# Kernel tuning notes

Hardware: AMD Instinct MI355X
Metric: run time of the kernel (lower is better)

The kernel has to match this reference:

```python
import jax, jax.numpy as jnp
import numpy as np

N_FLUID, N_BOX, K_MAX, KS, NCELL = 6000, 3000, 80, 4, 64
RADIUS = np.float32(0.5 * 1.5 * 6 * 0.025)  # filter_extent / 2 = 0.1125


def _ball_to_cube(p):
    """Volume-preserving ball->cube mapping (open3d ContinuousConv convention).
    p: [..., 3] coordinates in the unit ball; returns coords in [-1,1]^3."""
    eps = 1e-12
    x, y, z = p[..., 0], p[..., 1], p[..., 2]
    sq = x * x + y * y + z * z
    norm = jnp.sqrt(sq)
    rxy2 = x * x + y * y
    # sphere -> cylinder (volume preserving)
    polar = 1.25 * z * z > rxy2
    s_pol = jnp.sqrt(3.0 * norm / (norm + jnp.abs(z) + eps))
    s_eq = norm / jnp.sqrt(rxy2 + eps)
    xc = jnp.where(polar, s_pol * x, s_eq * x)
    yc = jnp.where(polar, s_pol * y, s_eq * y)
    zc = jnp.where(polar, jnp.sign(z) * norm, 1.5 * z * s_eq)
    zero = sq < 1e-12
    xc = jnp.where(zero, 0.0, xc)
    yc = jnp.where(zero, 0.0, yc)
    zc = jnp.where(zero, 0.0, zc)
    # cylinder -> cube (area-preserving disc -> square on xy)
    rxy = jnp.sqrt(xc * xc + yc * yc)
    FP = 4.0 / np.pi
    safe_x = jnp.where(jnp.abs(xc) < eps, eps, xc)
    safe_y = jnp.where(jnp.abs(yc) < eps, eps, yc)
    cond = jnp.abs(xc) >= jnp.abs(yc)
    u1 = jnp.sign(xc) * rxy
    v1 = u1 * FP * jnp.arctan(yc / safe_x)
    v2 = jnp.sign(yc) * rxy
    u2 = v2 * FP * jnp.arctan(xc / safe_y)
    u = jnp.where(cond, u1, u2)
    v = jnp.where(cond, v1, v2)
    small = rxy < eps
    u = jnp.where(small, 0.0, u)
    v = jnp.where(small, 0.0, v)
    return jnp.stack([u, v, zc], axis=-1)


def build_neighbors(pos_in, pos_out, ignore_self):
    """Fixed-radius neighbor search (capped at K_MAX) + window + trilinear
    interpolation cells/weights. Returns idx [No,K], cells [No,K,8] int32,
    coef [No,K,8] (trilinear weight * poly6 window * validity)."""
    d = pos_in[None, :, :] - pos_out[:, None, :]            # [No,Ni,3]
    d2 = jnp.sum(d * d, axis=-1)
    if ignore_self:
        ii = jnp.arange(pos_out.shape[0])
        d2 = jnp.where(ii[:, None] == ii[None, :], jnp.inf, d2)
    neg = jnp.where(d2 <= RADIUS * RADIUS, -d2, -jnp.inf)
    vals, idx = jax.lax.top_k(neg, K_MAX)                   # [No,K]
    valid = (vals > -jnp.inf).astype(pos_in.dtype)
    rel = (pos_in[idx] - pos_out[:, None, :]) / RADIUS      # [No,K,3] unit ball
    r2 = jnp.sum(rel * rel, axis=-1)
    win = jnp.clip((1.0 - r2) ** 3, 0.0, 1.0) * valid       # poly6 window
    g = jnp.clip((_ball_to_cube(rel) + 1.0) * 0.5 * (KS - 1), 0.0, KS - 1.0)
    i0 = jnp.clip(jnp.floor(g), 0, KS - 2).astype(jnp.int32)
    t = g - i0.astype(g.dtype)
    cells, tw = [], []
    for dx in (0, 1):
        for dy in (0, 1):
            for dz in (0, 1):
                w = ((t[..., 0] if dx else 1.0 - t[..., 0])
                     * (t[..., 1] if dy else 1.0 - t[..., 1])
                     * (t[..., 2] if dz else 1.0 - t[..., 2]))
                cell = ((i0[..., 2] + dz) * KS + (i0[..., 1] + dy)) * KS + (i0[..., 0] + dx)
                cells.append(cell)
                tw.append(w)
    cells = jnp.stack(cells, axis=-1)                       # [No,K,8]
    coef = jnp.stack(tw, axis=-1) * win[..., None]          # [No,K,8]
    return idx, cells, coef


def apply_cconv(feats_in, idx, cells, coef, W, b):
    """Continuous conv: scatter neighbor feats into 64 kernel cells per query,
    then contract with the filter. W: [64, F, O]."""
    N, K = idx.shape
    F = feats_in.shape[-1]
    nf = feats_in[idx]                                      # [N,K,F]
    S = jnp.zeros((N * NCELL, F), feats_in.dtype)
    row = (jnp.arange(N, dtype=jnp.int32) * NCELL)[:, None]
    for c in range(8):                                      # 8 trilinear corners
        flat = (row + cells[..., c]).reshape(-1)
        S = S.at[flat].add((coef[..., c:c + 1] * nf).reshape(-1, F))
    return jnp.einsum('ncf,cfo->no', S.reshape(N, NCELL, F), W) + b


def setup_inputs() -> dict:
    key = jax.random.key(0)
    ks = jax.random.split(key, 16)

    def p(i, shape, scale=0.05):
        return (scale * jax.random.normal(ks[i], shape)).astype(jnp.float32)

    return {
        'pos': jax.random.uniform(ks[0], (N_FLUID, 3), dtype=jnp.float32),
        'vel': jax.random.normal(ks[1], (N_FLUID, 3), dtype=jnp.float32),
        'box': jax.random.uniform(ks[2], (N_BOX, 3), dtype=jnp.float32),
        'box_feats': jax.random.normal(ks[3], (N_BOX, 3), dtype=jnp.float32),
        'cf_w': p(4, (NCELL, 4, 32)), 'cf_b': jnp.zeros((32,), jnp.float32),
        'co_w': p(5, (NCELL, 3, 32)), 'co_b': jnp.zeros((32,), jnp.float32),
        'd0_w': p(6, (4, 32)), 'd0_b': jnp.zeros((32,), jnp.float32),
        'c1_w': p(7, (NCELL, 96, 64)), 'c1_b': jnp.zeros((64,), jnp.float32),
        'd1_w': p(8, (96, 64)), 'd1_b': jnp.zeros((64,), jnp.float32),
        'c2_w': p(9, (NCELL, 64, 64)), 'c2_b': jnp.zeros((64,), jnp.float32),
        'd2_w': p(10, (64, 64)), 'd2_b': jnp.zeros((64,), jnp.float32),
        'c3_w': p(11, (NCELL, 64, 3)), 'c3_b': jnp.zeros((3,), jnp.float32),
        'd3_w': p(12, (64, 3)), 'd3_b': jnp.zeros((3,), jnp.float32),
    }


def reference(pos, vel, box, box_feats, cf_w, cf_b, co_w, co_b, d0_w, d0_b,
              c1_w, c1_b, d1_w, d1_b, c2_w, c2_b, d2_w, d2_b, c3_w, c3_b,
              d3_w, d3_b):
    fidx, fcells, fcoef = build_neighbors(pos, pos, True)
    oidx, ocells, ocoef = build_neighbors(box, pos, False)
    ff = jnp.concatenate([jnp.ones_like(pos[:, :1]), vel], axis=-1)  # [N,4]
    a_cf = apply_cconv(ff, fidx, fcells, fcoef, cf_w, cf_b)
    a_co = apply_cconv(box_feats, oidx, ocells, ocoef, co_w, co_b)
    a_d0 = ff @ d0_w + d0_b
    x = jnp.concatenate([a_co, a_cf, a_d0], axis=-1)                 # [N,96]
    for cw, cb, dw, db in ((c1_w, c1_b, d1_w, d1_b),
                           (c2_w, c2_b, d2_w, d2_b),
                           (c3_w, c3_b, d3_w, d3_b)):
        h = jax.nn.relu(x)
        y = apply_cconv(h, fidx, fcells, fcoef, cw, cb) + (h @ dw + db)
        x = y + x if y.shape[-1] == x.shape[-1] else y
    return x * (1.0 / 128.0)  # pos_correction [N,3]
```

## Files before the change

### kernel.cpp

```cpp
#include <hip/hip_runtime.h>
#include <math.h>

namespace {

constexpr int NQ  = 6000;
constexpr int NB  = 3000;
constexpr int K   = 80;
constexpr float RAD = 0.1125f;
constexpr float R2  = RAD * RAD;
constexpr float EPSF = 1e-12f;

constexpr int GS  = 8;
constexpr int NC  = GS*GS*GS;
constexpr int NO  = 65 * 64;
constexpr int NBLK = (NQ + 3) / 4;
constexpr int NBLK8 = ((NBLK + 7) / 8) * 8;
constexpr int PREPB = 512;

typedef __attribute__((ext_vector_type(8))) short bf16x8;
typedef __attribute__((ext_vector_type(4))) float f32x4;

__device__ __forceinline__ float sgn(float x) {
    return (x > 0.f) ? 1.f : ((x < 0.f) ? -1.f : 0.f);
}

__device__ __forceinline__ unsigned int bf16rne(float f) {
    unsigned int u = __float_as_uint(f);
    return (u + 0x7fffu + ((u >> 16) & 1u)) >> 16;
}
__device__ __forceinline__ float bf16f(unsigned short u) {
    return __uint_as_float(((unsigned int)u) << 16);
}
__device__ __forceinline__ int cell_of(float x, float y, float z) {
    int cx = min(max((int)(x * (float)GS), 0), GS-1);
    int cy = min(max((int)(y * (float)GS), 0), GS-1);
    int cz = min(max((int)(z * (float)GS), 0), GS-1);
    return (cz*GS + cy)*GS + cx;
}

__device__ void coef_store(float ddx, float ddy, float ddz, int slot,
                           int* __restrict__ cells, float* __restrict__ coefs)
{
    float rx = ddx / RAD, ry = ddy / RAD, rz = ddz / RAD;
    float r2 = rx*rx + ry*ry + rz*rz;
    float w1 = 1.f - r2;
    float win = (w1 > 0.f) ? w1*w1*w1 : 0.f;
    float norm = sqrtf(r2);
    float rxy2 = rx*rx + ry*ry;
    float xc, yc, zc;
    if (r2 < 1e-12f) {
        xc = yc = zc = 0.f;
    } else if (1.25f * rz * rz > rxy2) {
        float s = sqrtf(3.0f * norm / (norm + fabsf(rz) + EPSF));
        xc = s * rx; yc = s * ry; zc = sgn(rz) * norm;
    } else {
        float s = norm / sqrtf(rxy2 + EPSF);
        xc = s * rx; yc = s * ry; zc = 1.5f * rz * s;
    }
    float rxy = sqrtf(xc*xc + yc*yc);
    const float FP = (float)(4.0 / M_PI);
    float u, v;
    if (rxy < EPSF) {
        u = 0.f; v = 0.f;
    } else if (fabsf(xc) >= fabsf(yc)) {
        float sx = (fabsf(xc) < EPSF) ? EPSF : xc;
        u = sgn(xc) * rxy;
        v = u * FP * atanf(yc / sx);
    } else {
        float sy = (fabsf(yc) < EPSF) ? EPSF : yc;
        v = sgn(yc) * rxy;
        u = v * FP * atanf(xc / sy);
    }
    float gx = fminf(fmaxf((u  + 1.f) * 0.5f * 3.f, 0.f), 3.f);
    float gy = fminf(fmaxf((v  + 1.f) * 0.5f * 3.f, 0.f), 3.f);
    float gz = fminf(fmaxf((zc + 1.f) * 0.5f * 3.f, 0.f), 3.f);
    int ix = min((int)floorf(gx), 2);
    int iy = min((int)floorf(gy), 2);
    int iz = min((int)floorf(gz), 2);
    float tx = gx - (float)ix, ty = gy - (float)iy, tz = gz - (float)iz;
    cells[slot] = iz*16 + iy*4 + ix;
    float wx[2] = {1.f - tx, tx}, wy[2] = {1.f - ty, ty}, wz[2] = {1.f - tz, tz};
    float* cf = coefs + (size_t)slot * 8;
#pragma unroll
    for (int c = 0; c < 8; ++c)
        cf[c] = wx[c >> 2] * wy[(c >> 1) & 1] * wz[c & 1] * win;
}

__global__ __launch_bounds__(1024) void grid_build_kernel(
    const float* __restrict__ pos, const float* __restrict__ box,
    int* __restrict__ gs_f, int* __restrict__ gs_b,
    int* __restrict__ cur_f, int* __restrict__ cur_b)
{
    __shared__ int cntF[NC], cntB[NC];
    __shared__ int tmpF[NC], tmpB[NC];
    int tid = threadIdx.x;
    int half = tid >> 9, t = tid & 511;
    if (half == 0) cntF[t] = 0; else cntB[t] = 0;
    __syncthreads();
    for (int i = tid; i < NQ + NB; i += 1024) {
        if (i < NQ) {
            atomicAdd(&cntF[cell_of(pos[i*3], pos[i*3+1], pos[i*3+2])], 1);
        } else {
            int b = i - NQ;
            atomicAdd(&cntB[cell_of(box[b*3], box[b*3+1], box[b*3+2])], 1);
        }
    }
    __syncthreads();
    int* cnt = half ? cntB : cntF;
    int* tmp = half ? tmpB : tmpF;
    int cv = cnt[t];
    tmp[t] = cv;
    __syncthreads();
    for (int off = 1; off < NC; off <<= 1) {
        int v = (t >= off) ? tmp[t - off] : 0;
        __syncthreads();
        tmp[t] += v;
        __syncthreads();
    }
    int* gsd = half ? gs_b : gs_f;
    int* cur = half ? cur_b : cur_f;
    int excl = tmp[t] - cv;
    gsd[t] = excl;
    cur[t] = excl;
    if (t == NC - 1) gsd[NC] = tmp[t];
}

__global__ __launch_bounds__(256) void scatter_pts_kernel(
    const float* __restrict__ pos, const float* __restrict__ box,
    int* __restrict__ cur_f, int* __restrict__ cur_b,
    float* __restrict__ spf, int* __restrict__ sif,
    float* __restrict__ spb, int* __restrict__ sib)
{
    int t = blockIdx.x * blockDim.x + threadIdx.x;
    if (t < NQ) {
        float x = pos[t*3], y = pos[t*3+1], z = pos[t*3+2];
        int dst = atomicAdd(&cur_f[cell_of(x,y,z)], 1);
        spf[dst*3] = x; spf[dst*3+1] = y; spf[dst*3+2] = z;
        sif[dst] = t;
    } else if (t < NQ + NB) {
        int b = t - NQ;
        float x = box[b*3], y = box[b*3+1], z = box[b*3+2];
        int dst = atomicAdd(&cur_b[cell_of(x,y,z)], 1);
        spb[dst*3] = x; spb[dst*3+1] = y; spb[dst*3+2] = z;
        sib[dst] = b;
    }
}

__global__ __launch_bounds__(256) void nn2gc_kernel(
    const float* __restrict__ pos,
    const float* __restrict__ spf, const int* __restrict__ sif, const int* __restrict__ gsf,
    const float* __restrict__ spb, const int* __restrict__ sib, const int* __restrict__ gsb,
    int* __restrict__ f_cnt, int* __restrict__ f_idx, float* __restrict__ f_d2,
    int* __restrict__ f_cell, float* __restrict__ f_coef,
    int* __restrict__ b_cnt, int* __restrict__ b_idx, float* __restrict__ b_d2,
    int* __restrict__ b_cell, float* __restrict__ b_coef,
    const float* __restrict__ c1w, const float* __restrict__ d1w,
    const float* __restrict__ c2w, const float* __restrict__ d2w,
    const float* __restrict__ c3w, const float* __restrict__ d3w,
    const float* __restrict__ vel, const float* __restrict__ bfeat,
    const float* __restrict__ cfw, const float* __restrict__ cow,
    const float* __restrict__ d0w, const float* __restrict__ d0b,
    unsigned short* __restrict__ Bt1, unsigned short* __restrict__ Bt2,
    unsigned short* __restrict__ G0f, unsigned short* __restrict__ G0b,
    float* __restrict__ W3p, float* __restrict__ x1)
{
    if (blockIdx.x < PREPB) {
        int stride = PREPB * 256;
        int gid = blockIdx.x * 256 + threadIdx.x;
        for (int i = gid; i < NQ * 1024; i += stride) {
            int j = i >> 10, rr = i & 1023, c = rr >> 4, op = (rr & 15) * 2;
            float vx = vel[j*3+0], vy = vel[j*3+1], vz = vel[j*3+2];
            const float* w = cfw + (size_t)c * 128;
            float s0 = w[op]   + vx*w[32+op]   + vy*w[64+op]   + vz*w[96+op];
            float s1 = w[op+1] + vx*w[32+op+1] + vy*w[64+op+1] + vz*w[96+op+1];
            *reinterpret_cast<unsigned int*>(G0f + (size_t)j * 2048 + c*32 + op) =
                bf16rne(s0) | (bf16rne(s1) << 16);
        }
        for (int i = gid; i < NB * 1024; i += stride) {
            int j = i >> 10, rr = i & 1023, c = rr >> 4, op = (rr & 15) * 2;
            float b0 = bfeat[j*3+0], b1 = bfeat[j*3+1], b2 = bfeat[j*3+2];
            const float* w = cow + (size_t)c * 96;
            float s0 = b0*w[op]   + b1*w[32+op]   + b2*w[64+op];
            float s1 = b0*w[op+1] + b1*w[32+op+1] + b2*w[64+op+1];
            *reinterpret_cast<unsigned int*>(G0b + (size_t)j * 2048 + c*32 + op) =
                bf16rne(s0) | (bf16rne(s1) << 16);
        }
        for (int i = gid; i < NO * 96; i += stride) {
            int n = i / 96, f = i % 96, c = n >> 6, o = n & 63;
            float v = (c < 64) ? c1w[((size_t)c*96 + f)*64 + o] : d1w[f*64 + o];
            Bt1[i] = (unsigned short)bf16rne(v);
        }
        for (int i = gid; i < NO * 64; i += stride) {
            int n = i / 64, f = i % 64, c = n >> 6, o = n & 63;
            float v = (c < 64) ? c2w[((size_t)c*64 + f)*64 + o] : d2w[f*64 + o];
            Bt2[i] = (unsigned short)bf16rne(v);
        }
        for (int i = gid; i < 64 * 195; i += stride) {
            int f = i / 195, r = i % 195, c = r / 3, o = r % 3;
            W3p[i] = (c < 64) ? c3w[(c*64 + f)*3 + o] : d3w[f*3 + o];
        }
        for (int i = gid; i < NQ * 32; i += stride) {
            int n = i >> 5, o = i & 31;
            float acc = d0b[o] + d0w[o]
                      + vel[n*3+0] * d0w[32 + o]
                      + vel[n*3+1] * d0w[64 + o]
                      + vel[n*3+2] * d0w[96 + o];
            x1[n*96 + 64 + o] = acc;
        }
        return;
    }
    int gw = (int)(blockIdx.x - PREPB) * 4 + ((int)threadIdx.x >> 6);
    int lane = threadIdx.x & 63;
    if (gw >= 2 * NQ) return;
    bool isF = gw < NQ;
    int wid = isF ? gw : gw - NQ;
    const float* sp = isF ? spf : spb;
    const int*   si = isF ? sif : sib;
    const int*   gs = isF ? gsf : gsb;
    int*   cnt   = isF ? f_cnt  : b_cnt;
    int*   idxs  = isF ? f_idx  : b_idx;
    float* d2s   = isF ? f_d2   : b_d2;
    int*   cells = isF ? f_cell : b_cell;
    float* coefs = isF ? f_coef : b_coef;
    float qx = pos[wid*3+0], qy = pos[wid*3+1], qz = pos[wid*3+2];
    int cx = min(max((int)(qx * (float)GS), 0), GS-1);
    int cy = min(max((int)(qy * (float)GS), 0), GS-1);
    int cz = min(max((int)(qz * (float)GS), 0), GS-1);
    int x0 = max(cx-1, 0), x1c = min(cx+1, GS-1);
    int base = wid * K;
    int c = 0;
    for (int dz = -1; dz <= 1; ++dz) {
        int z = cz + dz; if ((unsigned)z >= (unsigned)GS) continue;
        for (int dy = -1; dy <= 1; ++dy) {
            int y = cy + dy; if ((unsigned)y >= (unsigned)GS) continue;
            int row = (z*GS + y)*GS;
            int s0 = gs[row + x0], s1 = gs[row + x1c + 1];
            for (int j0 = s0; j0 < s1; j0 += 64) {
                int ii = j0 + lane;
                float d2 = 1e30f; int oj = 0;
                float ddx = 0.f, ddy = 0.f, ddz = 0.f;
                if (ii < s1) {
                    oj = si[ii];
                    ddx = sp[ii*3+0]-qx; ddy = sp[ii*3+1]-qy; ddz = sp[ii*3+2]-qz;
                    d2 = ddx*ddx + ddy*ddy + ddz*ddz;
                    if (isF && oj == wid) d2 = 1e30f;
                }
                bool hit = d2 <= R2;
                unsigned long long m = __ballot(hit);
                int pc = __popcll(m);
                if (pc == 0) continue;
                if (c + pc <= K) {
                    if (hit) {
                        int p = c + __popcll(m & ((1ull << lane) - 1ull));
                        idxs[base + p] = oj;
                        d2s [base + p] = d2;
                        coef_store(ddx, ddy, ddz, base + p, cells, coefs);
                    }
                    c += pc;
                } else {
                    while (m) {
                        int l = __ffsll((unsigned long long)m) - 1;
                        m &= m - 1ull;
                        float dd = __shfl(d2, l);
                        int jv = __shfl(oj, l);
                        float ax = __shfl(ddx, l), ay = __shfl(ddy, l), az = __shfl(ddz, l);
                        int slot = -1;
                        if (c < K) { slot = c; c++; }
                        else {
                            float mx = -1.f; int am = 0;
                            for (int s = 0; s < K; ++s) {
                                float v = d2s[base + s];
                                if (v > mx) { mx = v; am = s; }
                            }
                            if (dd < mx) slot = am;
                        }
                        if (slot >= 0 && lane == 0) {
                            idxs[base + slot] = jv;
                            d2s [base + slot] = dd;
                            coef_store(ax, ay, az, base + slot, cells, coefs);
                        }
                    }
                }
            }
        }
    }
    if (lane == 0) cnt[wid] = c;
}

__global__ __launch_bounds__(256) void gather0_kernel(
    const int* __restrict__ order,
    const int* __restrict__ f_cnt, const int* __restrict__ f_idx,
    const int* __restrict__ f_cell, const float* __restrict__ f_coef,
    const int* __restrict__ b_cnt, const int* __restrict__ b_idx,
    const int* __restrict__ b_cell, const float* __restrict__ b_coef,
    const unsigned short* __restrict__ G0f, const unsigned short* __restrict__ G0b,
    const float* __restrict__ cfb, const float* __restrict__ cob,
    float* __restrict__ x1)
{
    __shared__ __align__(16) float coefF[K * 8];
    __shared__ __align__(16) float coefB[K * 8];
    __shared__ int jF[K], jB[K];
    __shared__ float partF[8][32], partB[8][32];
    int lb = (blockIdx.x & 7) * (gridDim.x >> 3) + (blockIdx.x >> 3);
    int tid = threadIdx.x;
    int wv = tid >> 6, lane = tid & 63;
    int h = lane >> 5, o = lane & 31;
    int r = wv * 2 + h;
    int n = order[lb];
    int cnf = f_cnt[n], cnb = b_cnt[n];
    {
        const float4* srcF = (const float4*)(f_coef + (size_t)n * K * 8);
        const float4* srcB = (const float4*)(b_coef + (size_t)n * K * 8);
        for (int i = tid; i < cnf * 2; i += 256) ((float4*)coefF)[i] = srcF[i];
        for (int i = tid; i < cnb * 2; i += 256) ((float4*)coefB)[i] = srcB[i];
        for (int i = tid; i < cnf; i += 256) jF[i] = f_idx[n*K + i] * 2048 + f_cell[n*K + i] * 32;
        for (int i = tid; i < cnb; i += 256) jB[i] = b_idx[n*K + i] * 2048 + b_cell[n*K + i] * 32;
    }
    __syncthreads();
    float af = 0.f;
#pragma unroll 2
    for (int k = r; k < cnf; k += 8) {
        const unsigned short* Gj = G0f + jF[k] + o;
        float4 cA = *reinterpret_cast<const float4*>(coefF + k*8);
        float4 cB = *reinterpret_cast<const float4*>(coefF + k*8 + 4);
        af += cA.x * bf16f(Gj[ 0 * 32]);
        af += cA.y * bf16f(Gj[16 * 32]);
        af += cA.z * bf16f(Gj[ 4 * 32]);
        af += cA.w * bf16f(Gj[20 * 32]);
        af += cB.x * bf16f(Gj[ 1 * 32]);
        af += cB.y * bf16f(Gj[17 * 32]);
        af += cB.z * bf16f(Gj[ 5 * 32]);
        af += cB.w * bf16f(Gj[21 * 32]);
    }
    float ab = 0.f;
#pragma unroll 2
    for (int k = r; k < cnb; k += 8) {
        const unsigned short* Gj = G0b + jB[k] + o;
        float4 cA = *reinterpret_cast<const float4*>(coefB + k*8);
        float4 cB = *reinterpret_cast<const float4*>(coefB + k*8 + 4);
        ab += cA.x * bf16f(Gj[ 0 * 32]);
        ab += cA.y * bf16f(Gj[16 * 32]);
        ab += cA.z * bf16f(Gj[ 4 * 32]);
        ab += cA.w * bf16f(Gj[20 * 32]);
        ab += cB.x * bf16f(Gj[ 1 * 32]);
        ab += cB.y * bf16f(Gj[17 * 32]);
        ab += cB.z * bf16f(Gj[ 5 * 32]);
        ab += cB.w * bf16f(Gj[21 * 32]);
    }
    partF[r][o] = af;
    partB[r][o] = ab;
    __syncthreads();
    if (tid < 64) {
        int oo = tid & 31;
        if (tid < 32) {
            float s = cfb[oo];
#pragma unroll
            for (int q = 0; q < 8; ++q) s += partF[q][oo];
            x1[(size_t)n * 96 + 32 + oo] = s;
        } else {
            float s = cob[oo];
#pragma unroll
            for (int q = 0; q < 8; ++q) s += partB[q][oo];
            x1[(size_t)n * 96 + oo] = s;
        }
    }
}

template<int F>
__global__ __launch_bounds__(256) void gemmGm_kernel(
    const float* __restrict__ feats,
    const unsigned short* __restrict__ Bt,
    unsigned short* __restrict__ G,
    int M)
{
    constexpr int NT = 5;
    constexpr int AST = F + 8;
    __shared__ unsigned short As[64 * AST];
    __shared__ unsigned short Bs[64 * AST];
    int tid = threadIdx.x, lane = tid & 63, wv = tid >> 6;
    int m0 = blockIdx.x * 64;
    int nt0 = blockIdx.y * NT;
    for (int i = tid; i < 64 * F / 4; i += 256) {
        int m = i / (F / 4), k4 = i % (F / 4);
        int gm = m0 + m; if (gm >= M) gm = M - 1;
        float4 av = *reinterpret_cast<const float4*>(feats + (size_t)gm * F + k4 * 4);
        uint2 ov;
        ov.x = bf16rne(fmaxf(av.x, 0.f)) | (bf16rne(fmaxf(av.y, 0.f)) << 16);
        ov.y = bf16rne(fmaxf(av.z, 0.f)) | (bf16rne(fmaxf(av.w, 0.f)) << 16);
        *reinterpret_cast<uint2*>(As + m * AST + k4 * 4) = ov;
    }
    int mr = lane & 15, quad = lane >> 4;
    for (int t = 0; t < NT; ++t) {
        int no0 = (nt0 + t) * 64;
        __syncthreads();
        for (int i = tid; i < 64 * F / 8; i += 256) {
            int nn = i / (F / 8), k8 = i % (F / 8);
            *reinterpret_cast<uint4*>(Bs + nn * AST + k8 * 8) =
                *reinterpret_cast<const uint4*>(Bt + (size_t)(no0 + nn) * F + k8 * 8);
        }
        __syncthreads();
        f32x4 acc[4] = {{0.f,0.f,0.f,0.f},{0.f,0.f,0.f,0.f},
                        {0.f,0.f,0.f,0.f},{0.f,0.f,0.f,0.f}};
#pragma unroll
        for (int kc = 0; kc < F; kc += 32) {
            bf16x8 a = *reinterpret_cast<const bf16x8*>(As + (wv*16 + mr) * AST + kc + quad*8);
#pragma unroll
            for (int q = 0; q < 4; ++q) {
                bf16x8 b = *reinterpret_cast<const bf16x8*>(Bs + (q*16 + mr) * AST + kc + quad*8);
                acc[q] = __builtin_amdgcn_mfma_f32_16x16x32_bf16(a, b, acc[q], 0, 0, 0);
            }
        }
#pragma unroll
        for (int q = 0; q < 4; ++q) {
#pragma unroll
            for (int rr = 0; rr < 4; ++rr) {
                int gm = m0 + wv*16 + quad*4 + rr;
                if (gm < M)
                    G[(size_t)gm * NO + no0 + q*16 + mr] = (unsigned short)bf16rne(acc[q][rr]);
            }
        }
    }
}

template<int FUSEY>
__global__ __launch_bounds__(256) void gatherG_kernel(
    const int* __restrict__ order,
    const int* __restrict__ cnt, const int* __restrict__ nidx,
    const int* __restrict__ ncell, const float* __restrict__ ncoef,
    const unsigned short* __restrict__ G,
    const float* __restrict__ cb, const float* __restrict__ db,
    const float* __restrict__ resid, float* __restrict__ out,
    const float* __restrict__ W3p, float* __restrict__ Y)
{
    __shared__ __align__(16) float coefL[K * 8];
    __shared__ int jL[K];
    __shared__ float part[3][64];
    __shared__ float xs[64];
    int lb = (blockIdx.x & 7) * (gridDim.x >> 3) + (blockIdx.x >> 3);
    int tid = threadIdx.x;
    int wv = tid >> 6, lane = tid & 63;
    int n = order[lb];
    int cn = cnt[n];
    {
        const float4* src = (const float4*)(ncoef + (size_t)n * K * 8);
        float4* dst = (float4*)coefL;
        for (int i = tid; i < cn * 2; i += 256) dst[i] = src[i];
        for (int i = tid; i < cn; i += 256)
            jL[i] = nidx[n*K + i] * NO + ncell[n*K + i] * 64;
    }
    __syncthreads();
    float a0 = 0.f, a1 = 0.f, a2 = 0.f, a3 = 0.f;
#pragma unroll 2
    for (int k = wv; k < cn; k += 4) {
        float4 cA = *reinterpret_cast<const float4*>(coefL + k*8);
        float4 cB = *reinterpret_cast<const float4*>(coefL + k*8 + 4);
        const unsigned short* Gj = G + jL[k] + lane;
        a0 += cA.x * bf16f(Gj[ 0 * 64]);
        a1 += cA.y * bf16f(Gj[16 * 64]);
        a2 += cA.z * bf16f(Gj[ 4 * 64]);
        a3 += cA.w * bf16f(Gj[20 * 64]);
        a0 += cB.x * bf16f(Gj[ 1 * 64]);
        a1 += cB.y * bf16f(Gj[17 * 64]);
        a2 += cB.z * bf16f(Gj[ 5 * 64]);
        a3 += cB.w * bf16f(Gj[21 * 64]);
    }
    float s = (a0 + a1) + (a2 + a3);
    if (wv > 0) part[wv - 1][lane] = s;
    __syncthreads();
    if (wv == 0) {
        float acc = cb[lane] + db[lane] + s
                  + part[0][lane] + part[1][lane] + part[2][lane];
        acc += bf16f(G[(size_t)n * NO + 64*64 + lane]);
        if (resid) acc += resid[(size_t)n * 64 + lane];
        if (!FUSEY) {
            out[(size_t)n * 64 + lane] = acc;
        } else {
            xs[lane] = fmaxf(acc, 0.f);
        }
    }
    if (FUSEY) {
        __syncthreads();
        for (int t = tid; t < 195; t += 256) {
            float sum = 0.f;
#pragma unroll 16
            for (int f = 0; f < 64; ++f) sum += xs[f] * W3p[f*195 + t];
            Y[(size_t)n * 195 + t] = sum;
        }
    }
}

__global__ __launch_bounds__(256) void gather3_kernel(
    const int* __restrict__ order,
    const int* __restrict__ cnt, const int* __restrict__ nidx,
    const int* __restrict__ ncell, const float* __restrict__ ncoef,
    const float* __restrict__ Y,
    const float* __restrict__ cb3, const float* __restrict__ db3,
    float* __restrict__ out)
{
    int lb = (blockIdx.x & 7) * (gridDim.x >> 3) + (blockIdx.x >> 3);
    int gw = lb * 4 + ((int)threadIdx.x >> 6);
    int lane = threadIdx.x & 63;
    if (gw >= NQ) return;
    int n = order[gw];
    int cn = cnt[n];
    float a0 = 0.f, a1 = 0.f, a2 = 0.f;
#pragma unroll
    for (int seg = 0; seg < 2; ++seg) {
        int kidx = seg * 64 + lane;
        if (kidx < cn) {
            int j  = nidx [n*K + kidx];
            int cb = ncell[n*K + kidx];
            const float* cf = ncoef + (size_t)(n*K + kidx) * 8;
            const float* Yj = Y + (size_t)j * 195;
#pragma unroll
            for (int c = 0; c < 8; ++c) {
                int cell = cb + (c & 1)*16 + ((c >> 1) & 1)*4 + (c >> 2);
                float wgt = cf[c];
                const float* Tp = Yj + cell*3;
                a0 += wgt * Tp[0];
                a1 += wgt * Tp[1];
                a2 += wgt * Tp[2];
            }
        }
    }
#pragma unroll
    for (int s = 32; s > 0; s >>= 1) {
        a0 += __shfl_down(a0, s);
        a1 += __shfl_down(a1, s);
        a2 += __shfl_down(a2, s);
    }
    if (lane == 0) {
        const float* Yn = Y + (size_t)n * 195 + 192;
        out[n*3+0] = (a0 + Yn[0] + cb3[0] + db3[0]) * (1.f/128.f);
        out[n*3+1] = (a1 + Yn[1] + cb3[1] + db3[1]) * (1.f/128.f);
        out[n*3+2] = (a2 + Yn[2] + cb3[2] + db3[2]) * (1.f/128.f);
    }
}

}

extern "C" void kernel_launch(void* const* d_in, const int* in_sizes, int n_in,
                              void* d_out, int out_size, void* d_ws, size_t ws_size,
                              hipStream_t stream)
{
    const float* pos       = (const float*)d_in[0];
    const float* vel       = (const float*)d_in[1];
    const float* box       = (const float*)d_in[2];
    const float* box_feats = (const float*)d_in[3];
    const float* cf_w = (const float*)d_in[4];  const float* cf_b = (const float*)d_in[5];
    const float* co_w = (const float*)d_in[6];  const float* co_b = (const float*)d_in[7];
    const float* d0_w = (const float*)d_in[8];  const float* d0_b = (const float*)d_in[9];
    const float* c1_w = (const float*)d_in[10]; const float* c1_b = (const float*)d_in[11];
    const float* d1_w = (const float*)d_in[12]; const float* d1_b = (const float*)d_in[13];
    const float* c2_w = (const float*)d_in[14]; const float* c2_b = (const float*)d_in[15];
    const float* d2_w = (const float*)d_in[16]; const float* d2_b = (const float*)d_in[17];
    const float* c3_w = (const float*)d_in[18]; const float* c3_b = (const float*)d_in[19];
    const float* d3_w = (const float*)d_in[20]; const float* d3_b = (const float*)d_in[21];

    char* wsb = (char*)d_ws;
    size_t off = 0;
    auto alloc = [&](size_t bytes) {
        void* p = wsb + off;
        off = (off + bytes + 255) & ~(size_t)255;
        return p;
    };
    char*  Graw = (char*)alloc((size_t)NQ * NO * 2 + 4096);
    unsigned short* G = (unsigned short*)Graw;
    float* f_d2 = (float*)Graw;
    float* b_d2 = (float*)Graw + (size_t)NQ * K;
    unsigned short* G0f = (unsigned short*)(Graw + ((size_t)4 << 20));
    unsigned short* G0b = (unsigned short*)(Graw + ((size_t)32 << 20));
    int*   f_cnt  = (int*)  alloc((size_t)NQ * 4);
    int*   f_idx  = (int*)  alloc((size_t)NQ * K * 4);
    int*   f_cell = (int*)  alloc((size_t)NQ * K * 4);
    float* f_coef = (float*)alloc((size_t)NQ * K * 8 * 4);
    int*   b_cnt  = (int*)  alloc((size_t)NQ * 4);
    int*   b_idx  = (int*)  alloc((size_t)NQ * K * 4);
    int*   b_cell = (int*)  alloc((size_t)NQ * K * 4);
    float* b_coef = (float*)alloc((size_t)NQ * K * 8 * 4);
    float* x1     = (float*)alloc((size_t)NQ * 96 * 4);
    float* x2     = (float*)alloc((size_t)NQ * 64 * 4);
    unsigned short* Bt1 = (unsigned short*)alloc((size_t)NO * 96 * 2);
    unsigned short* Bt2 = (unsigned short*)alloc((size_t)NO * 64 * 2);
    float* W3p    = (float*)alloc((size_t)64 * 195 * 4);
    float* Y      = (float*)alloc((size_t)NQ * 195 * 4);
    int*   gs_f   = (int*)  alloc((size_t)(NC + 1) * 4);
    int*   gs_b   = (int*)  alloc((size_t)(NC + 1) * 4);
    int*   cur_f  = (int*)  alloc((size_t)NC * 4);
    int*   cur_b  = (int*)  alloc((size_t)NC * 4);
    float* spf    = (float*)alloc((size_t)NQ * 3 * 4);
    int*   sif    = (int*)  alloc((size_t)NQ * 4);
    float* spb    = (float*)alloc((size_t)NB * 3 * 4);
    int*   sib    = (int*)  alloc((size_t)NB * 4);

    dim3 b256(256);
    grid_build_kernel<<<1, 1024, 0, stream>>>(pos, box, gs_f, gs_b, cur_f, cur_b);
    scatter_pts_kernel<<<(NQ + NB + 255)/256, b256, 0, stream>>>(
        pos, box, cur_f, cur_b, spf, sif, spb, sib);
    nn2gc_kernel<<<PREPB + (2*NQ + 3)/4, b256, 0, stream>>>(
        pos, spf, sif, gs_f, spb, sib, gs_b,
        f_cnt, f_idx, f_d2, f_cell, f_coef,
        b_cnt, b_idx, b_d2, b_cell, b_coef,
        c1_w, d1_w, c2_w, d2_w, c3_w, d3_w,
        vel, box_feats, cf_w, co_w, d0_w, d0_b,
        Bt1, Bt2, G0f, G0b, W3p, x1);
    gather0_kernel<<<NQ, b256, 0, stream>>>(sif,
        f_cnt, f_idx, f_cell, f_coef,
        b_cnt, b_idx, b_cell, b_coef,
        G0f, G0b, cf_b, co_b, x1);
    gemmGm_kernel<96><<<dim3((NQ+63)/64, 13), b256, 0, stream>>>(x1, Bt1, G, NQ);
    gatherG_kernel<0><<<NQ, b256, 0, stream>>>(sif, f_cnt, f_idx, f_cell, f_coef,
        G, c1_b, d1_b, nullptr, x2, nullptr, nullptr);
    gemmGm_kernel<64><<<dim3((NQ+63)/64, 13), b256, 0, stream>>>(x2, Bt2, G, NQ);
    gatherG_kernel<1><<<NQ, b256, 0, stream>>>(sif, f_cnt, f_idx, f_cell, f_coef,
        G, c2_b, d2_b, x2, nullptr, W3p, Y);
    gather3_kernel<<<NBLK8, b256, 0, stream>>>(sif, f_cnt, f_idx, f_cell, f_coef,
        Y, c3_b, d3_b, (float*)d_out);

    (void)in_sizes; (void)n_in; (void)out_size; (void)ws_size;
    (void)f_d2; (void)b_d2;
}
```

Measured before the change: 255.2 us.

## Defer coefficient computation to a lane-parallel pass after neighbor search

The neighbor search no longer computes the ball-to-cube mapping and trilinear coefficients inline, where it ran divergently on only the hit lanes (or only lane 0 in the overflow path). It now stores raw displacements into the coef slots and then runs the coefficient computation in a dense pass over all found neighbours, one neighbour per lane. Sorted point positions are padded to float4 so each is read with a single vector load, division by the radius becomes multiplication by its reciprocal, and coefficients are written as two float4 stores. The extra pass re-reads the stored displacements from global memory, and the reciprocal multiply can differ from the division in the last bit.

```diff
diff --git a/kernel.cpp b/kernel.cpp
--- a/kernel.cpp
+++ b/kernel.cpp
@@ -7,6 +7,7 @@
 constexpr int NB  = 3000;
 constexpr int K   = 80;
 constexpr float RAD = 0.1125f;
+constexpr float RADI = 1.0f / 0.1125f;
 constexpr float R2  = RAD * RAD;
 constexpr float EPSF = 1e-12f;
 
@@ -38,10 +39,11 @@
     return (cz*GS + cy)*GS + cx;
 }
 
-__device__ void coef_store(float ddx, float ddy, float ddz, int slot,
-                           int* __restrict__ cells, float* __restrict__ coefs)
-{
-    float rx = ddx / RAD, ry = ddy / RAD, rz = ddz / RAD;
+__device__ __forceinline__ void coef_compute(
+    float ddx, float ddy, float ddz, int slot,
+    int* __restrict__ cells, float* __restrict__ coefs)
+{
+    float rx = ddx * RADI, ry = ddy * RADI, rz = ddz * RADI;
     float r2 = rx*rx + ry*ry + rz*rz;
     float w1 = 1.f - r2;
     float win = (w1 > 0.f) ? w1*w1*w1 : 0.f;
@@ -79,11 +81,18 @@
     int iz = min((int)floorf(gz), 2);
     float tx = gx - (float)ix, ty = gy - (float)iy, tz = gz - (float)iz;
     cells[slot] = iz*16 + iy*4 + ix;
-    float wx[2] = {1.f - tx, tx}, wy[2] = {1.f - ty, ty}, wz[2] = {1.f - tz, tz};
-    float* cf = coefs + (size_t)slot * 8;
-#pragma unroll
-    for (int c = 0; c < 8; ++c)
-        cf[c] = wx[c >> 2] * wy[(c >> 1) & 1] * wz[c & 1] * win;
+    float wx0 = 1.f - tx, wy0 = 1.f - ty, wz0 = 1.f - tz;
+    float4 lo, hi;
+    lo.x = wx0 * wy0 * wz0 * win;
+    lo.y = wx0 * wy0 * tz  * win;
+    lo.z = wx0 * ty  * wz0 * win;
+    lo.w = wx0 * ty  * tz  * win;
+    hi.x = tx  * wy0 * wz0 * win;
+    hi.y = tx  * wy0 * tz  * win;
+    hi.z = tx  * ty  * wz0 * win;
+    hi.w = tx  * ty  * tz  * win;
+    float4* cf = (float4*)(coefs + (size_t)slot * 8);
+    cf[0] = lo; cf[1] = hi;
 }
 
 __global__ __launch_bounds__(1024) void grid_build_kernel(
@@ -135,13 +144,13 @@
     if (t < NQ) {
         float x = pos[t*3], y = pos[t*3+1], z = pos[t*3+2];
         int dst = atomicAdd(&cur_f[cell_of(x,y,z)], 1);
-        spf[dst*3] = x; spf[dst*3+1] = y; spf[dst*3+2] = z;
+        *reinterpret_cast<float4*>(spf + (size_t)dst*4) = make_float4(x, y, z, 0.f);
         sif[dst] = t;
     } else if (t < NQ + NB) {
         int b = t - NQ;
         float x = box[b*3], y = box[b*3+1], z = box[b*3+2];
         int dst = atomicAdd(&cur_b[cell_of(x,y,z)], 1);
-        spb[dst*3] = x; spb[dst*3+1] = y; spb[dst*3+2] = z;
+        *reinterpret_cast<float4*>(spb + (size_t)dst*4) = make_float4(x, y, z, 0.f);
         sib[dst] = b;
     }
 }
@@ -241,7 +250,8 @@
                 float ddx = 0.f, ddy = 0.f, ddz = 0.f;
                 if (ii < s1) {
                     oj = si[ii];
-                    ddx = sp[ii*3+0]-qx; ddy = sp[ii*3+1]-qy; ddz = sp[ii*3+2]-qz;
+                    float4 p = *reinterpret_cast<const float4*>(sp + (size_t)ii*4);
+                    ddx = p.x - qx; ddy = p.y - qy; ddz = p.z - qz;
                     d2 = ddx*ddx + ddy*ddy + ddz*ddz;
                     if (isF && oj == wid) d2 = 1e30f;
                 }
@@ -254,7 +264,8 @@
                         int p = c + __popcll(m & ((1ull << lane) - 1ull));
                         idxs[base + p] = oj;
                         d2s [base + p] = d2;
-                        coef_store(ddx, ddy, ddz, base + p, cells, coefs);
+                        float* cf = coefs + (size_t)(base + p) * 8;
+                        cf[0] = ddx; cf[1] = ddy; cf[2] = ddz;
                     }
                     c += pc;
                 } else {
@@ -277,12 +288,17 @@
                         if (slot >= 0 && lane == 0) {
                             idxs[base + slot] = jv;
                             d2s [base + slot] = dd;
-                            coef_store(ax, ay, az, base + slot, cells, coefs);
+                            float* cf = coefs + (size_t)(base + slot) * 8;
+                            cf[0] = ax; cf[1] = ay; cf[2] = az;
                         }
                     }
                 }
             }
         }
+    }
+    for (int k2 = lane; k2 < c; k2 += 64) {
+        const float4 d = *reinterpret_cast<const float4*>(coefs + (size_t)(base + k2) * 8);
+        coef_compute(d.x, d.y, d.z, base + k2, cells, coefs);
     }
     if (lane == 0) cnt[wid] = c;
 }
@@ -588,9 +604,9 @@
     int*   gs_b   = (int*)  alloc((size_t)(NC + 1) * 4);
     int*   cur_f  = (int*)  alloc((size_t)NC * 4);
     int*   cur_b  = (int*)  alloc((size_t)NC * 4);
-    float* spf    = (float*)alloc((size_t)NQ * 3 * 4);
+    float* spf    = (float*)alloc((size_t)NQ * 4 * 4);
     int*   sif    = (int*)  alloc((size_t)NQ * 4);
-    float* spb    = (float*)alloc((size_t)NB * 3 * 4);
+    float* spb    = (float*)alloc((size_t)NB * 4 * 4);
     int*   sib    = (int*)  alloc((size_t)NB * 4);
 
     dim3 b256(256);
```

New measurement: 243.8 us. 1.05x faster.
